# Performance work log

Measured on AMD Instinct MI355X. Metric: run time of the kernel, lower is better.

The kernel has to match this reference:

```python
import jax, jax.numpy as jnp
import numpy as np

DIM, HEADS, K = 128, 4, 7
HD = DIM // HEADS


def _nbr_idx(n, k):
    # NATTEN boundary-clamped neighborhood (dilation=1): window start clamped to [0, n-k]
    i = np.arange(n)
    start = np.clip(i - k // 2, 0, n - k)
    idx = start[:, None] + np.arange(k)[None, :]          # (n, k) absolute neighbor index
    rel = idx - i[:, None] + (k - 1)                      # (n, k) index into 2k-1 rpb axis
    return jnp.asarray(idx), jnp.asarray(rel)


def _ln(x, w, b, eps=1e-5):
    mu = jnp.mean(x, -1, keepdims=True)
    var = jnp.var(x, -1, keepdims=True)
    return (x - mu) * jax.lax.rsqrt(var + eps) * w + b


def setup_inputs() -> dict:
    key = jax.random.key(0)
    ks = jax.random.split(key, 16)
    B, H, W, C = 1, 128, 128, DIM
    f = jax.random.normal
    inp = {
        'x': f(ks[0], (B, H, W, C), jnp.float32),
        'y': f(ks[1], (B, H, W, C), jnp.float32),
        'qv_w': f(ks[2], (2 * C, C), jnp.float32) * 0.02,
        'qv_b': jnp.zeros((2 * C,), jnp.float32),
        'k_w': f(ks[3], (C, C), jnp.float32) * 0.02,
        'k_b': jnp.zeros((C,), jnp.float32),
        'rpb': f(ks[4], (HEADS, 2 * K - 1, 2 * K - 1), jnp.float32) * 0.02,
        'proj_w': f(ks[5], (C, C), jnp.float32) * 0.02,
        'proj_b': jnp.zeros((C,), jnp.float32),
        'n1_w': jnp.ones((C,), jnp.float32),
        'n1_b': jnp.zeros((C,), jnp.float32),
        'n2_w': jnp.ones((C,), jnp.float32),
        'n2_b': jnp.zeros((C,), jnp.float32),
        'fc1_w': f(ks[6], (4 * C, C), jnp.float32) * 0.02,
        'fc1_b': jnp.zeros((4 * C,), jnp.float32),
        'fc2_w': f(ks[7], (C, 4 * C), jnp.float32) * 0.02,
        'fc2_b': jnp.zeros((C,), jnp.float32),
    }
    return inp


def _block(x, y, qv_w, qv_b, k_w, k_b, rpb, proj_w, proj_b,
           n1_w, n1_b, n2_w, n2_b, fc1_w, fc1_b, fc2_w, fc2_b):
    B, H, W, C = x.shape
    scale = HD ** -0.5
    # ---- CrossNat2D attention on norm1(x) vs y ----
    xn = _ln(x, n1_w, n1_b)
    qv = xn @ qv_w.T + qv_b                               # (B,H,W,2C)
    q = qv[..., :C].reshape(B, H, W, HEADS, HD) * scale
    v = qv[..., C:].reshape(B, H, W, HEADS, HD)
    k = (y @ k_w.T + k_b).reshape(B, H, W, HEADS, HD)

    idx_h, rel_h = _nbr_idx(H, K)
    idx_w, rel_w = _nbr_idx(W, K)
    # gather neighborhoods: (B, H, K, W, K, HEADS, HD)
    k_nbr = k[:, idx_h][:, :, :, idx_w]
    v_nbr = v[:, idx_h][:, :, :, idx_w]

    # attention logits over KxK neighborhood
    attn = jnp.einsum('bijhd,biajchd->bijhac', q, k_nbr)  # (B,H,W,heads,K,K)
    bias = rpb[:, rel_h][..., rel_w]                      # (heads,H,K,W,K)
    attn = attn + jnp.transpose(bias, (1, 3, 0, 2, 4))    # broadcast over B
    attn = jax.nn.softmax(attn.reshape(B, H, W, HEADS, K * K), axis=-1)
    attn = attn.reshape(B, H, W, HEADS, K, K)

    out = jnp.einsum('bijhac,biajchd->bijhd', attn, v_nbr).reshape(B, H, W, C)
    out = out @ proj_w.T + proj_b

    x = x + out
    # ---- MLP ----
    h = _ln(x, n2_w, n2_b) @ fc1_w.T + fc1_b
    h = jax.nn.gelu(h, approximate=False) @ fc2_w.T + fc2_b
    return x + h


def reference(x, y, qv_w, qv_b, k_w, k_b, rpb, proj_w, proj_b,
              n1_w, n1_b, n2_w, n2_b, fc1_w, fc1_b, fc2_w, fc2_b):
    return _block(x, y, qv_w, qv_b, k_w, k_b, rpb, proj_w, proj_b,
                  n1_w, n1_b, n2_w, n2_b, fc1_w, fc1_b, fc2_w, fc2_b)
```

## Files before the change

### kernel.cpp

```cpp
#include <hip/hip_runtime.h>
#include <hip/hip_bf16.h>


#define N_PIX 16384
#define C 128
#define HEADS 4
#define HD 32
#define HW 128

typedef __hip_bfloat16 bf16;
typedef __attribute__((ext_vector_type(8))) short bf16x8;
typedef __attribute__((ext_vector_type(4))) float f32x4;

__device__ __forceinline__ short f2bs(float f) {
    unsigned int r;
    asm("v_cvt_pk_bf16_f32 %0, %1, %2" : "=v"(r) : "v"(f), "v"(f));
    return (short)(r & 0xffff);
}
__device__ __forceinline__ unsigned int pack2(float a, float b) {
    unsigned int r;
    asm("v_cvt_pk_bf16_f32 %0, %1, %2" : "=v"(r) : "v"(a), "v"(b));
    return r;
}
__device__ __forceinline__ float bs2f(short s) {
    __hip_bfloat16_raw r; r.x = (unsigned short)s;
    return __bfloat162float(__hip_bfloat16(r));
}
__device__ __forceinline__ float gelu_f(float v) {
    const float z2 = v * (2.302236206f + 0.102943322f * v * v);
    return v / (1.f + exp2f(-z2));
}

__global__ __launch_bounds__(256) void k_wconv(
    const float* __restrict__ qv_w, const float* __restrict__ k_w,
    const float* __restrict__ proj_w, const float* __restrict__ fc1_w,
    const float* __restrict__ fc2_w,
    short* __restrict__ wqv, short* __restrict__ wk, short* __restrict__ wproj,
    short* __restrict__ wfc1, short* __restrict__ wfc2) {
    const int i = blockIdx.x * 256 + threadIdx.x;
    if (i < 32768) wqv[i] = f2bs(qv_w[i]);
    if (i < 16384) { wk[i] = f2bs(k_w[i]); wproj[i] = f2bs(proj_w[i]); }
    if (i < 65536) { wfc1[i] = f2bs(fc1_w[i]); wfc2[i] = f2bs(fc2_w[i]); }
}

__global__ __launch_bounds__(256, 4) void k_qkv(
    const float* __restrict__ x, const float* __restrict__ y,
    const short* __restrict__ wqv, const float* __restrict__ qv_b,
    const short* __restrict__ wk, const float* __restrict__ k_b,
    const float* __restrict__ n1_w, const float* __restrict__ n1_b,
    bf16* __restrict__ qb, bf16* __restrict__ vb, bf16* __restrict__ kb) {
    __shared__ short xn[16][136];
    __shared__ short yl[16][136];
    const int t = threadIdx.x;
    const int pix0 = (blockIdx.x & 7) * 2048 + (blockIdx.x >> 3) * 16;
    {
        const int r = t >> 4, ch8 = (t & 15) * 8;
        const size_t gp = (size_t)(pix0 + r) * C + ch8;
        float xv[8], yv[8];
        *(float4*)&xv[0] = *(const float4*)(x + gp);
        *(float4*)&xv[4] = *(const float4*)(x + gp + 4);
        *(float4*)&yv[0] = *(const float4*)(y + gp);
        *(float4*)&yv[4] = *(const float4*)(y + gp + 4);
        float sm = 0.f, sq = 0.f;
#pragma unroll
        for (int i2 = 0; i2 < 8; i2++) { sm += xv[i2]; sq += xv[i2] * xv[i2]; }
#pragma unroll
        for (int msk = 1; msk < 16; msk <<= 1) {
            sm += __shfl_xor(sm, msk, 64); sq += __shfl_xor(sq, msk, 64);
        }
        const float mu = sm * (1.f / 128.f);
        const float ri = rsqrtf(sq * (1.f / 128.f) - mu * mu + 1e-5f);
        float w1[8], b1[8];
        *(float4*)&w1[0] = *(const float4*)(n1_w + ch8);
        *(float4*)&w1[4] = *(const float4*)(n1_w + ch8 + 4);
        *(float4*)&b1[0] = *(const float4*)(n1_b + ch8);
        *(float4*)&b1[4] = *(const float4*)(n1_b + ch8 + 4);
        uint4 xp, yp;
        xp.x = pack2((xv[0] - mu) * ri * w1[0] + b1[0], (xv[1] - mu) * ri * w1[1] + b1[1]);
        xp.y = pack2((xv[2] - mu) * ri * w1[2] + b1[2], (xv[3] - mu) * ri * w1[3] + b1[3]);
        xp.z = pack2((xv[4] - mu) * ri * w1[4] + b1[4], (xv[5] - mu) * ri * w1[5] + b1[5]);
        xp.w = pack2((xv[6] - mu) * ri * w1[6] + b1[6], (xv[7] - mu) * ri * w1[7] + b1[7]);
        yp.x = pack2(yv[0], yv[1]); yp.y = pack2(yv[2], yv[3]);
        yp.z = pack2(yv[4], yv[5]); yp.w = pack2(yv[6], yv[7]);
        *(uint4*)&xn[r][ch8] = xp;
        *(uint4*)&yl[r][ch8] = yp;
    }
    __syncthreads();
    const int wave = t >> 6, lane = t & 63, quad = lane >> 4, l15 = lane & 15;
    const float scale = 0.1767766952966369f;
    {
        bf16x8 aA[4];
#pragma unroll
        for (int kt = 0; kt < 4; kt++)
            aA[kt] = *(const bf16x8*)&xn[l15][kt * 32 + quad * 8];
#pragma unroll
        for (int s = 0; s < 4; s++) {
            const int n = (wave + 4 * s) * 16 + l15;
            f32x4 acc = {0.f, 0.f, 0.f, 0.f};
#pragma unroll
            for (int kt = 0; kt < 4; kt++) {
                bf16x8 b = *(const bf16x8*)&wqv[n * C + kt * 32 + quad * 8];
                acc = __builtin_amdgcn_mfma_f32_16x16x32_bf16(aA[kt], b, acc, 0, 0, 0);
            }
            const float bias = qv_b[n];
#pragma unroll
            for (int r = 0; r < 4; r++) {
                const int m = quad * 4 + r;
                const float v = acc[r] + bias;
                if (s < 2) qb[(size_t)(pix0 + m) * C + n] = __float2bfloat16(v * scale);
                else       vb[(size_t)(pix0 + m) * C + (n - C)] = __float2bfloat16(v);
            }
        }
    }
    {
        bf16x8 aY[4];
#pragma unroll
        for (int kt = 0; kt < 4; kt++)
            aY[kt] = *(const bf16x8*)&yl[l15][kt * 32 + quad * 8];
        const int n0 = (wave * 2) * 16 + l15, n1 = (wave * 2 + 1) * 16 + l15;
        f32x4 a0 = {0.f, 0.f, 0.f, 0.f}, a1 = {0.f, 0.f, 0.f, 0.f};
#pragma unroll
        for (int kt = 0; kt < 4; kt++) {
            bf16x8 b0 = *(const bf16x8*)&wk[n0 * C + kt * 32 + quad * 8];
            bf16x8 b1 = *(const bf16x8*)&wk[n1 * C + kt * 32 + quad * 8];
            a0 = __builtin_amdgcn_mfma_f32_16x16x32_bf16(aY[kt], b0, a0, 0, 0, 0);
            a1 = __builtin_amdgcn_mfma_f32_16x16x32_bf16(aY[kt], b1, a1, 0, 0, 0);
        }
        const float b0s = k_b[n0], b1s = k_b[n1];
#pragma unroll
        for (int r = 0; r < 4; r++) {
            const int m = quad * 4 + r;
            kb[(size_t)(pix0 + m) * C + n0] = __float2bfloat16(a0[r] + b0s);
            kb[(size_t)(pix0 + m) * C + n1] = __float2bfloat16(a1[r] + b1s);
        }
    }
}

__global__ __launch_bounds__(512, 2) void k_fam(
    const bf16* __restrict__ qb, const bf16* __restrict__ kb,
    const bf16* __restrict__ vb, const float* __restrict__ rpb,
    const float* __restrict__ x,
    const short* __restrict__ wproj, const float* __restrict__ proj_b,
    const float* __restrict__ n2_w, const float* __restrict__ n2_b,
    const short* __restrict__ wfc1, const float* __restrict__ fc1_b,
    const short* __restrict__ wfc2, const float* __restrict__ fc2_b,
    float* __restrict__ out) {
    __shared__ short SH[67104];
    short* const KU  = SH;
    short* const VU  = SH + 25872;
    short* const Pb  = SH + 51744;
    short* const aoL = SH;
    short* const xnb = SH + 8448;
    short* const hb  = SH + 16896;
    short* const x1b = SH + 51744;
    const int t = threadIdx.x;
    const int wave = t >> 6, lane = t & 63, quad = lane >> 4, l15 = lane & 15;
    const int h = wave & 3, mt = wave >> 2;
    const int p = wave & 1, g = wave >> 1;
    const int tile = (blockIdx.x & 7) * 32 + (blockIdx.x >> 3);
    const int i0 = (tile >> 4) * 8, j0 = (tile & 15) * 8;
    const int rs = min(max(i0 - 3, 0), 114);
    const int cs2 = min(max(j0 - 3, 0), 114);
    const int n_0 = (2 * g) * 16 + l15, n_1 = (2 * g + 1) * 16 + l15;
    bf16x8 aQv[2];
#pragma unroll
    for (int u = 0; u < 2; u++) {
        const int q = mt * 2 + u;
        const int iq = i0 + (q >> 1) * 4, jq = j0 + (q & 1) * 4;
        const int pA = (iq + (l15 >> 2)) * HW + jq + (l15 & 3);
        aQv[u] = *(const bf16x8*)(qb + (size_t)pA * C + h * HD + quad * 8);
    }
    float xres[2][2][4];
#pragma unroll
    for (int u = 0; u < 2; u++) {
        const int qm = 2 * p + u;
        const int ib = i0 + (qm >> 1) * 4 + quad, jb = j0 + (qm & 1) * 4;
#pragma unroll
        for (int r = 0; r < 4; r++) {
            const size_t pp = (size_t)(ib * HW + jb + r) * C;
            xres[u][0][r] = x[pp + n_0];
            xres[u][1][r] = x[pp + n_1];
        }
    }
    {
        const int seg = t & 15, r0 = t >> 4;
        int q14 = (r0 >= 28) ? 2 : (r0 >= 14 ? 1 : 0);
        int m14 = r0 - 14 * q14;
        int r = r0;
#pragma unroll
        for (int it = 0; it < 7; it++) {
            if (r < 196) {
                const size_t gp = (size_t)((rs + q14) * HW + (cs2 + m14)) * C + seg * 8;
                *(uint4*)&KU[r * 132 + seg * 8] = *(const uint4*)(kb + gp);
                *(uint4*)&VU[r * 132 + seg * 8] = *(const uint4*)(vb + gp);
            }
            r += 32; q14 += 2; m14 += 4;
            if (m14 >= 14) { m14 -= 14; q14 += 1; }
        }
    }
    int nrA[7], ncA[7];
    {
        int nr = (l15 >= 10) ? 1 : 0;
        int nc = l15 - ((l15 >= 10) ? 10 : 0);
#pragma unroll
        for (int nt = 0; nt < 7; nt++) {
            nrA[nt] = nr; ncA[nt] = nc;
            nc += 6; nr += 1;
            if (nc >= 10) { nc -= 10; nr += 1; }
        }
    }
    __syncthreads();
    const float* rpbh = rpb + h * 169;
    f32x4 Oacc[2][2];
#pragma unroll
    for (int u = 0; u < 2; u++) {
        Oacc[u][0] = (f32x4){0.f, 0.f, 0.f, 0.f};
        Oacc[u][1] = (f32x4){0.f, 0.f, 0.f, 0.f};
    }
#pragma unroll
    for (int u = 0; u < 2; u++) {
        const int q = mt * 2 + u;
        const int iq = i0 + (q >> 1) * 4, jq = j0 + (q & 1) * 4;
        const int rq = min(max(iq - 3, 0), 118), cq = min(max(jq - 3, 0), 118);
        const int vbase = (rq - rs) * 14 + (cq - cs2);
        f32x4 S[7];
#pragma unroll
        for (int nt = 0; nt < 7; nt++) {
            const int lr = min(vbase + nrA[nt] * 14 + ncA[nt], 195);
            const bf16x8 bK = *(const bf16x8*)&KU[lr * 132 + h * HD + quad * 8];
            f32x4 z = {0.f, 0.f, 0.f, 0.f};
            S[nt] = __builtin_amdgcn_mfma_f32_16x16x32_bf16(aQv[u], bK, z, 0, 0, 0);
        }
        float smx[4];
#pragma unroll
        for (int r = 0; r < 4; r++) {
            const int i = iq + quad, j = jq + r;
            const int shi = min(max(i - 3, 0), 121);
            const int swj = min(max(j - 3, 0), 121);
            float best = -1e30f;
#pragma unroll
            for (int nt = 0; nt < 7; nt++) {
                const int ai = rq + nrA[nt], aj = cq + ncA[nt];
                const bool vnb = (nt < 6) | (l15 < 4);
                const bool valid = vnb & (ai >= shi) & (ai <= shi + 6) & (aj >= swj) & (aj <= swj + 6);
                const int ri = min(max(ai - i + 6, 0), 12);
                const int rj = min(max(aj - j + 6, 0), 12);
                const float v = valid ? (S[nt][r] + rpbh[ri * 13 + rj]) : -1e30f;
                S[nt][r] = v;
                best = fmaxf(best, v);
            }
            for (int msk = 1; msk < 16; msk <<= 1) best = fmaxf(best, __shfl_xor(best, msk, 64));
            float s = 0.f;
#pragma unroll
            for (int nt = 0; nt < 7; nt++) {
                const float e = __expf(S[nt][r] - best);
                S[nt][r] = e;
                s += e;
            }
            for (int msk = 1; msk < 16; msk <<= 1) s += __shfl_xor(s, msk, 64);
            smx[r] = 1.f / s;
        }
#pragma unroll
        for (int r = 0; r < 4; r++) {
            short* prow = &Pb[(wave * 16 + quad * 4 + r) * 120];
#pragma unroll
            for (int nt = 0; nt < 7; nt++)
                prow[nt * 16 + l15] = f2bs(S[nt][r] * smx[r]);
        }
#pragma unroll
        for (int kt = 0; kt < 3; kt++) {
            const bf16x8 aP = *(const bf16x8*)&Pb[(wave * 16 + l15) * 120 + kt * 32 + quad * 8];
            const int kbase = kt * 32 + quad * 8;
            int kr = (kbase * 205) >> 11;
            int kc = kbase - 10 * kr;
            int sidx = vbase + kr * 14 + kc;
            int lvr[8];
#pragma unroll
            for (int jj = 0; jj < 8; jj++) {
                lvr[jj] = sidx;
                kc++; sidx++;
                if (kc >= 10) { kc = 0; sidx += 4; }
            }
#pragma unroll
            for (int nt2 = 0; nt2 < 2; nt2++) {
                const int ch = h * HD + nt2 * 16 + l15;
                bf16x8 bV;
#pragma unroll
                for (int jj = 0; jj < 8; jj++) bV[jj] = VU[lvr[jj] * 132 + ch];
                Oacc[u][nt2] = __builtin_amdgcn_mfma_f32_16x16x32_bf16(aP, bV, Oacc[u][nt2], 0, 0, 0);
            }
        }
        {
            bf16x8 aP = {0, 0, 0, 0, 0, 0, 0, 0};
            if (quad < 2) aP = *(const bf16x8*)&Pb[(wave * 16 + l15) * 120 + 96 + quad * 8];
#pragma unroll
            for (int nt2 = 0; nt2 < 2; nt2++) {
                const int ch = h * HD + nt2 * 16 + l15;
                bf16x8 bV = {0, 0, 0, 0, 0, 0, 0, 0};
                if (quad == 0) {
#pragma unroll
                    for (int jj = 0; jj < 8; jj++) {
                        const int kc3 = (6 + jj > 9) ? 9 : 6 + jj;
                        bV[jj] = VU[(vbase + 126 + kc3) * 132 + ch];
                    }
                }
                Oacc[u][nt2] = __builtin_amdgcn_mfma_f32_16x16x32_bf16(aP, bV, Oacc[u][nt2], 0, 0, 0);
            }
        }
    }
    bf16x8 wp0[4], wp1[4];
#pragma unroll
    for (int kt = 0; kt < 4; kt++) {
        wp0[kt] = *(const bf16x8*)&wproj[n_0 * C + kt * 32 + quad * 8];
        wp1[kt] = *(const bf16x8*)&wproj[n_1 * C + kt * 32 + quad * 8];
    }
    __syncthreads();
#pragma unroll
    for (int u = 0; u < 2; u++) {
        const int q = mt * 2 + u;
#pragma unroll
        for (int r = 0; r < 4; r++) {
            const int m = q * 16 + quad * 4 + r;
            aoL[m * 132 + h * HD + l15] = f2bs(Oacc[u][0][r]);
            aoL[m * 132 + h * HD + 16 + l15] = f2bs(Oacc[u][1][r]);
        }
    }
    __syncthreads();
    float x1f[2][2][4];
    {
        bf16x8 aO[2][4];
#pragma unroll
        for (int u = 0; u < 2; u++)
#pragma unroll
            for (int kt = 0; kt < 4; kt++)
                aO[u][kt] = *(const bf16x8*)&aoL[((2 * p + u) * 16 + l15) * 132 + kt * 32 + quad * 8];
        f32x4 pa[2][2];
        pa[0][0] = (f32x4){0.f, 0.f, 0.f, 0.f}; pa[0][1] = (f32x4){0.f, 0.f, 0.f, 0.f};
        pa[1][0] = (f32x4){0.f, 0.f, 0.f, 0.f}; pa[1][1] = (f32x4){0.f, 0.f, 0.f, 0.f};
#pragma unroll
        for (int kt = 0; kt < 4; kt++) {
            pa[0][0] = __builtin_amdgcn_mfma_f32_16x16x32_bf16(aO[0][kt], wp0[kt], pa[0][0], 0, 0, 0);
            pa[0][1] = __builtin_amdgcn_mfma_f32_16x16x32_bf16(aO[0][kt], wp1[kt], pa[0][1], 0, 0, 0);
            pa[1][0] = __builtin_amdgcn_mfma_f32_16x16x32_bf16(aO[1][kt], wp0[kt], pa[1][0], 0, 0, 0);
            pa[1][1] = __builtin_amdgcn_mfma_f32_16x16x32_bf16(aO[1][kt], wp1[kt], pa[1][1], 0, 0, 0);
        }
        const float b0s = proj_b[n_0], b1s = proj_b[n_1];
#pragma unroll
        for (int u = 0; u < 2; u++) {
#pragma unroll
            for (int r = 0; r < 4; r++) {
                const int m = (2 * p + u) * 16 + quad * 4 + r;
                const float v0 = xres[u][0][r] + pa[u][0][r] + b0s;
                const float v1 = xres[u][1][r] + pa[u][1][r] + b1s;
                x1f[u][0][r] = v0; x1f[u][1][r] = v1;
                x1b[m * 132 + n_0] = f2bs(v0);
                x1b[m * 132 + n_1] = f2bs(v1);
            }
        }
    }
    __syncthreads();
    {
        const int row = t >> 3, c16 = (t & 7) * 16;
        float xv[16];
        {
            const uint4 d0 = *(const uint4*)&x1b[row * 132 + c16];
            const uint4 d1 = *(const uint4*)&x1b[row * 132 + c16 + 8];
            const unsigned int w[8] = {d0.x, d0.y, d0.z, d0.w, d1.x, d1.y, d1.z, d1.w};
#pragma unroll
            for (int i2 = 0; i2 < 8; i2++) {
                xv[2 * i2]     = bs2f((short)(w[i2] & 0xffff));
                xv[2 * i2 + 1] = bs2f((short)(w[i2] >> 16));
            }
        }
        float sm = 0.f, sq = 0.f;
#pragma unroll
        for (int i2 = 0; i2 < 16; i2++) { sm += xv[i2]; sq += xv[i2] * xv[i2]; }
#pragma unroll
        for (int msk = 1; msk < 8; msk <<= 1) {
            sm += __shfl_xor(sm, msk, 64); sq += __shfl_xor(sq, msk, 64);
        }
        const float mu = sm * (1.f / 128.f);
        const float ri = rsqrtf(sq * (1.f / 128.f) - mu * mu + 1e-5f);
        float w2[16], b2[16];
        *(float4*)&w2[0]  = *(const float4*)(n2_w + c16);
        *(float4*)&w2[4]  = *(const float4*)(n2_w + c16 + 4);
        *(float4*)&w2[8]  = *(const float4*)(n2_w + c16 + 8);
        *(float4*)&w2[12] = *(const float4*)(n2_w + c16 + 12);
        *(float4*)&b2[0]  = *(const float4*)(n2_b + c16);
        *(float4*)&b2[4]  = *(const float4*)(n2_b + c16 + 4);
        *(float4*)&b2[8]  = *(const float4*)(n2_b + c16 + 8);
        *(float4*)&b2[12] = *(const float4*)(n2_b + c16 + 12);
        uint4 o0, o1;
        o0.x = pack2((xv[0] - mu) * ri * w2[0] + b2[0],   (xv[1] - mu) * ri * w2[1] + b2[1]);
        o0.y = pack2((xv[2] - mu) * ri * w2[2] + b2[2],   (xv[3] - mu) * ri * w2[3] + b2[3]);
        o0.z = pack2((xv[4] - mu) * ri * w2[4] + b2[4],   (xv[5] - mu) * ri * w2[5] + b2[5]);
        o0.w = pack2((xv[6] - mu) * ri * w2[6] + b2[6],   (xv[7] - mu) * ri * w2[7] + b2[7]);
        o1.x = pack2((xv[8] - mu) * ri * w2[8] + b2[8],   (xv[9] - mu) * ri * w2[9] + b2[9]);
        o1.y = pack2((xv[10] - mu) * ri * w2[10] + b2[10], (xv[11] - mu) * ri * w2[11] + b2[11]);
        o1.z = pack2((xv[12] - mu) * ri * w2[12] + b2[12], (xv[13] - mu) * ri * w2[13] + b2[13]);
        o1.w = pack2((xv[14] - mu) * ri * w2[14] + b2[14], (xv[15] - mu) * ri * w2[15] + b2[15]);
        *(uint4*)&xnb[row * 132 + c16] = o0;
        *(uint4*)&xnb[row * 132 + c16 + 8] = o1;
    }
    __syncthreads();
    {
        bf16x8 aX[2][4];
#pragma unroll
        for (int u = 0; u < 2; u++)
#pragma unroll
            for (int kt = 0; kt < 4; kt++)
                aX[u][kt] = *(const bf16x8*)&xnb[((2 * p + u) * 16 + l15) * 132 + kt * 32 + quad * 8];
#pragma unroll
        for (int a = 0; a < 8; a++) {
            const int n = (g * 8 + a) * 16 + l15;
            f32x4 c0 = {0.f, 0.f, 0.f, 0.f}, c1 = {0.f, 0.f, 0.f, 0.f};
#pragma unroll
            for (int kt = 0; kt < 4; kt++) {
                const bf16x8 bw = *(const bf16x8*)&wfc1[n * C + kt * 32 + quad * 8];
                c0 = __builtin_amdgcn_mfma_f32_16x16x32_bf16(aX[0][kt], bw, c0, 0, 0, 0);
                c1 = __builtin_amdgcn_mfma_f32_16x16x32_bf16(aX[1][kt], bw, c1, 0, 0, 0);
            }
            const float bias = fc1_b[n];
#pragma unroll
            for (int r = 0; r < 4; r++) {
                const int m0 = (2 * p) * 16 + quad * 4 + r;
                hb[m0 * 520 + n] = f2bs(gelu_f(c0[r] + bias));
                hb[(m0 + 16) * 520 + n] = f2bs(gelu_f(c1[r] + bias));
            }
        }
    }
    __syncthreads();
    {
        f32x4 f00 = {0.f, 0.f, 0.f, 0.f}, f01 = {0.f, 0.f, 0.f, 0.f};
        f32x4 f10 = {0.f, 0.f, 0.f, 0.f}, f11 = {0.f, 0.f, 0.f, 0.f};
#pragma unroll
        for (int kt = 0; kt < 16; kt++) {
            const bf16x8 a0 = *(const bf16x8*)&hb[((2 * p) * 16 + l15) * 520 + kt * 32 + quad * 8];
            const bf16x8 a1 = *(const bf16x8*)&hb[((2 * p + 1) * 16 + l15) * 520 + kt * 32 + quad * 8];
            const bf16x8 w0 = *(const bf16x8*)&wfc2[n_0 * 512 + kt * 32 + quad * 8];
            const bf16x8 w1 = *(const bf16x8*)&wfc2[n_1 * 512 + kt * 32 + quad * 8];
            f00 = __builtin_amdgcn_mfma_f32_16x16x32_bf16(a0, w0, f00, 0, 0, 0);
            f01 = __builtin_amdgcn_mfma_f32_16x16x32_bf16(a0, w1, f01, 0, 0, 0);
            f10 = __builtin_amdgcn_mfma_f32_16x16x32_bf16(a1, w0, f10, 0, 0, 0);
            f11 = __builtin_amdgcn_mfma_f32_16x16x32_bf16(a1, w1, f11, 0, 0, 0);
        }
        const float b0s = fc2_b[n_0], b1s = fc2_b[n_1];
#pragma unroll
        for (int u = 0; u < 2; u++) {
            const int qm = 2 * p + u;
            const int ib = i0 + (qm >> 1) * 4 + quad, jb = j0 + (qm & 1) * 4;
#pragma unroll
            for (int r = 0; r < 4; r++) {
                const size_t pp = (size_t)(ib * HW + jb + r) * C;
                const float v0 = (u ? f10[r] : f00[r]) + b0s + x1f[u][0][r];
                const float v1 = (u ? f11[r] : f01[r]) + b1s + x1f[u][1][r];
                out[pp + n_0] = v0;
                out[pp + n_1] = v1;
            }
        }
    }
}

extern "C" void kernel_launch(void* const* d_in, const int* in_sizes, int n_in,
                              void* d_out, int out_size, void* d_ws, size_t ws_size,
                              hipStream_t stream) {
    const float* x      = (const float*)d_in[0];
    const float* y      = (const float*)d_in[1];
    const float* qv_w   = (const float*)d_in[2];
    const float* qv_b   = (const float*)d_in[3];
    const float* k_w    = (const float*)d_in[4];
    const float* k_b    = (const float*)d_in[5];
    const float* rpb    = (const float*)d_in[6];
    const float* proj_w = (const float*)d_in[7];
    const float* proj_b = (const float*)d_in[8];
    const float* n1_w   = (const float*)d_in[9];
    const float* n1_b   = (const float*)d_in[10];
    const float* n2_w   = (const float*)d_in[11];
    const float* n2_b   = (const float*)d_in[12];
    const float* fc1_w  = (const float*)d_in[13];
    const float* fc1_b  = (const float*)d_in[14];
    const float* fc2_w  = (const float*)d_in[15];
    const float* fc2_b  = (const float*)d_in[16];
    float* out = (float*)d_out;

    bf16* qb  = (bf16*)d_ws;
    bf16* vb  = qb + (size_t)N_PIX * C;
    bf16* kb  = vb + (size_t)N_PIX * C;
    short* wqv  = (short*)(kb + (size_t)N_PIX * C);
    short* wk   = wqv + 32768;
    short* wproj= wk + 16384;
    short* wfc1 = wproj + 16384;
    short* wfc2 = wfc1 + 65536;

    k_wconv<<<256, 256, 0, stream>>>(qv_w, k_w, proj_w, fc1_w, fc2_w,
                                     wqv, wk, wproj, wfc1, wfc2);
    k_qkv<<<1024, 256, 0, stream>>>(x, y, wqv, qv_b, wk, k_b, n1_w, n1_b,
                                    qb, vb, kb);
    k_fam<<<256, 512, 0, stream>>>(qb, kb, vb, rpb, x, wproj, proj_b, n2_w, n2_b,
                                   wfc1, fc1_b, wfc2, fc2_b, out);
}
```

Before: 152.6 us.

## Enlarge QKV projection tile to 64 pixels per block with register weight reuse

The QKV kernel now processes 64 pixels per 512-thread block instead of 16 per 256 threads. Each wave loads its weight column fragments once and reuses them across four 16-row M tiles, which cuts redundant global weight loads per pixel. Grid size drops from 1024 to 256 blocks, so there are fewer waves to hide latency and register pressure rises from holding 16 A-fragments per wave.

```diff
diff --git a/kernel.cpp b/kernel.cpp
--- a/kernel.cpp
+++ b/kernel.cpp
@@ -43,96 +43,134 @@
     if (i < 65536) { wfc1[i] = f2bs(fc1_w[i]); wfc2[i] = f2bs(fc2_w[i]); }
 }
 
-__global__ __launch_bounds__(256, 4) void k_qkv(
+__global__ __launch_bounds__(512, 4) void k_qkv(
     const float* __restrict__ x, const float* __restrict__ y,
     const short* __restrict__ wqv, const float* __restrict__ qv_b,
     const short* __restrict__ wk, const float* __restrict__ k_b,
     const float* __restrict__ n1_w, const float* __restrict__ n1_b,
     bf16* __restrict__ qb, bf16* __restrict__ vb, bf16* __restrict__ kb) {
-    __shared__ short xn[16][136];
-    __shared__ short yl[16][136];
+    __shared__ short xn[64][136];
+    __shared__ short yl[64][136];
     const int t = threadIdx.x;
-    const int pix0 = (blockIdx.x & 7) * 2048 + (blockIdx.x >> 3) * 16;
-    {
-        const int r = t >> 4, ch8 = (t & 15) * 8;
-        const size_t gp = (size_t)(pix0 + r) * C + ch8;
-        float xv[8], yv[8];
-        *(float4*)&xv[0] = *(const float4*)(x + gp);
-        *(float4*)&xv[4] = *(const float4*)(x + gp + 4);
-        *(float4*)&yv[0] = *(const float4*)(y + gp);
-        *(float4*)&yv[4] = *(const float4*)(y + gp + 4);
+    const int pix0 = ((blockIdx.x & 7) * 32 + (blockIdx.x >> 3)) * 64;
+    {
+        const int r = t >> 3, c16 = (t & 7) * 16;
+        const size_t gp = (size_t)(pix0 + r) * C + c16;
+        float xv[16], yv[16];
+        *(float4*)&xv[0]  = *(const float4*)(x + gp);
+        *(float4*)&xv[4]  = *(const float4*)(x + gp + 4);
+        *(float4*)&xv[8]  = *(const float4*)(x + gp + 8);
+        *(float4*)&xv[12] = *(const float4*)(x + gp + 12);
+        *(float4*)&yv[0]  = *(const float4*)(y + gp);
+        *(float4*)&yv[4]  = *(const float4*)(y + gp + 4);
+        *(float4*)&yv[8]  = *(const float4*)(y + gp + 8);
+        *(float4*)&yv[12] = *(const float4*)(y + gp + 12);
         float sm = 0.f, sq = 0.f;
 #pragma unroll
-        for (int i2 = 0; i2 < 8; i2++) { sm += xv[i2]; sq += xv[i2] * xv[i2]; }
-#pragma unroll
-        for (int msk = 1; msk < 16; msk <<= 1) {
+        for (int i2 = 0; i2 < 16; i2++) { sm += xv[i2]; sq += xv[i2] * xv[i2]; }
+#pragma unroll
+        for (int msk = 1; msk < 8; msk <<= 1) {
             sm += __shfl_xor(sm, msk, 64); sq += __shfl_xor(sq, msk, 64);
         }
         const float mu = sm * (1.f / 128.f);
         const float ri = rsqrtf(sq * (1.f / 128.f) - mu * mu + 1e-5f);
-        float w1[8], b1[8];
-        *(float4*)&w1[0] = *(const float4*)(n1_w + ch8);
-        *(float4*)&w1[4] = *(const float4*)(n1_w + ch8 + 4);
-        *(float4*)&b1[0] = *(const float4*)(n1_b + ch8);
-        *(float4*)&b1[4] = *(const float4*)(n1_b + ch8 + 4);
-        uint4 xp, yp;
-        xp.x = pack2((xv[0] - mu) * ri * w1[0] + b1[0], (xv[1] - mu) * ri * w1[1] + b1[1]);
-        xp.y = pack2((xv[2] - mu) * ri * w1[2] + b1[2], (xv[3] - mu) * ri * w1[3] + b1[3]);
-        xp.z = pack2((xv[4] - mu) * ri * w1[4] + b1[4], (xv[5] - mu) * ri * w1[5] + b1[5]);
-        xp.w = pack2((xv[6] - mu) * ri * w1[6] + b1[6], (xv[7] - mu) * ri * w1[7] + b1[7]);
-        yp.x = pack2(yv[0], yv[1]); yp.y = pack2(yv[2], yv[3]);
-        yp.z = pack2(yv[4], yv[5]); yp.w = pack2(yv[6], yv[7]);
-        *(uint4*)&xn[r][ch8] = xp;
-        *(uint4*)&yl[r][ch8] = yp;
+        float w1[16], b1[16];
+        *(float4*)&w1[0]  = *(const float4*)(n1_w + c16);
+        *(float4*)&w1[4]  = *(const float4*)(n1_w + c16 + 4);
+        *(float4*)&w1[8]  = *(const float4*)(n1_w + c16 + 8);
+        *(float4*)&w1[12] = *(const float4*)(n1_w + c16 + 12);
+        *(float4*)&b1[0]  = *(const float4*)(n1_b + c16);
+        *(float4*)&b1[4]  = *(const float4*)(n1_b + c16 + 4);
+        *(float4*)&b1[8]  = *(const float4*)(n1_b + c16 + 8);
+        *(float4*)&b1[12] = *(const float4*)(n1_b + c16 + 12);
+        uint4 o0, o1, p0, p1;
+        o0.x = pack2((xv[0] - mu) * ri * w1[0] + b1[0],   (xv[1] - mu) * ri * w1[1] + b1[1]);
+        o0.y = pack2((xv[2] - mu) * ri * w1[2] + b1[2],   (xv[3] - mu) * ri * w1[3] + b1[3]);
+        o0.z = pack2((xv[4] - mu) * ri * w1[4] + b1[4],   (xv[5] - mu) * ri * w1[5] + b1[5]);
+        o0.w = pack2((xv[6] - mu) * ri * w1[6] + b1[6],   (xv[7] - mu) * ri * w1[7] + b1[7]);
+        o1.x = pack2((xv[8] - mu) * ri * w1[8] + b1[8],   (xv[9] - mu) * ri * w1[9] + b1[9]);
+        o1.y = pack2((xv[10] - mu) * ri * w1[10] + b1[10], (xv[11] - mu) * ri * w1[11] + b1[11]);
+        o1.z = pack2((xv[12] - mu) * ri * w1[12] + b1[12], (xv[13] - mu) * ri * w1[13] + b1[13]);
+        o1.w = pack2((xv[14] - mu) * ri * w1[14] + b1[14], (xv[15] - mu) * ri * w1[15] + b1[15]);
+        p0.x = pack2(yv[0], yv[1]);   p0.y = pack2(yv[2], yv[3]);
+        p0.z = pack2(yv[4], yv[5]);   p0.w = pack2(yv[6], yv[7]);
+        p1.x = pack2(yv[8], yv[9]);   p1.y = pack2(yv[10], yv[11]);
+        p1.z = pack2(yv[12], yv[13]); p1.w = pack2(yv[14], yv[15]);
+        *(uint4*)&xn[r][c16] = o0;
+        *(uint4*)&xn[r][c16 + 8] = o1;
+        *(uint4*)&yl[r][c16] = p0;
+        *(uint4*)&yl[r][c16 + 8] = p1;
     }
     __syncthreads();
     const int wave = t >> 6, lane = t & 63, quad = lane >> 4, l15 = lane & 15;
     const float scale = 0.1767766952966369f;
     {
-        bf16x8 aA[4];
+        bf16x8 aA[4][4];
+#pragma unroll
+        for (int m = 0; m < 4; m++)
+#pragma unroll
+            for (int kt = 0; kt < 4; kt++)
+                aA[m][kt] = *(const bf16x8*)&xn[m * 16 + l15][kt * 32 + quad * 8];
+#pragma unroll
+        for (int s = 0; s < 2; s++) {
+            const int n = (wave * 2 + s) * 16 + l15;
+            bf16x8 w[4];
+#pragma unroll
+            for (int kt = 0; kt < 4; kt++)
+                w[kt] = *(const bf16x8*)&wqv[n * C + kt * 32 + quad * 8];
+            f32x4 acc[4];
+#pragma unroll
+            for (int m = 0; m < 4; m++) acc[m] = (f32x4){0.f, 0.f, 0.f, 0.f};
+#pragma unroll
+            for (int m = 0; m < 4; m++)
+#pragma unroll
+                for (int kt = 0; kt < 4; kt++)
+                    acc[m] = __builtin_amdgcn_mfma_f32_16x16x32_bf16(aA[m][kt], w[kt], acc[m], 0, 0, 0);
+            const float bias = qv_b[n];
+            if (wave * 2 + s < 8) {
+#pragma unroll
+                for (int m = 0; m < 4; m++)
+#pragma unroll
+                    for (int r = 0; r < 4; r++)
+                        qb[(size_t)(pix0 + m * 16 + quad * 4 + r) * C + n] =
+                            __float2bfloat16((acc[m][r] + bias) * scale);
+            } else {
+#pragma unroll
+                for (int m = 0; m < 4; m++)
+#pragma unroll
+                    for (int r = 0; r < 4; r++)
+                        vb[(size_t)(pix0 + m * 16 + quad * 4 + r) * C + (n - C)] =
+                            __float2bfloat16(acc[m][r] + bias);
+            }
+        }
+    }
+    {
+        bf16x8 aY[4][4];
+#pragma unroll
+        for (int m = 0; m < 4; m++)
+#pragma unroll
+            for (int kt = 0; kt < 4; kt++)
+                aY[m][kt] = *(const bf16x8*)&yl[m * 16 + l15][kt * 32 + quad * 8];
+        const int n = wave * 16 + l15;
+        bf16x8 w[4];
 #pragma unroll
         for (int kt = 0; kt < 4; kt++)
-            aA[kt] = *(const bf16x8*)&xn[l15][kt * 32 + quad * 8];
-#pragma unroll
-        for (int s = 0; s < 4; s++) {
-            const int n = (wave + 4 * s) * 16 + l15;
-            f32x4 acc = {0.f, 0.f, 0.f, 0.f};
-#pragma unroll
-            for (int kt = 0; kt < 4; kt++) {
-                bf16x8 b = *(const bf16x8*)&wqv[n * C + kt * 32 + quad * 8];
-                acc = __builtin_amdgcn_mfma_f32_16x16x32_bf16(aA[kt], b, acc, 0, 0, 0);
-            }
-            const float bias = qv_b[n];
-#pragma unroll
-            for (int r = 0; r < 4; r++) {
-                const int m = quad * 4 + r;
-                const float v = acc[r] + bias;
-                if (s < 2) qb[(size_t)(pix0 + m) * C + n] = __float2bfloat16(v * scale);
-                else       vb[(size_t)(pix0 + m) * C + (n - C)] = __float2bfloat16(v);
-            }
-        }
-    }
-    {
-        bf16x8 aY[4];
-#pragma unroll
-        for (int kt = 0; kt < 4; kt++)
-            aY[kt] = *(const bf16x8*)&yl[l15][kt * 32 + quad * 8];
-        const int n0 = (wave * 2) * 16 + l15, n1 = (wave * 2 + 1) * 16 + l15;
-        f32x4 a0 = {0.f, 0.f, 0.f, 0.f}, a1 = {0.f, 0.f, 0.f, 0.f};
-#pragma unroll
-        for (int kt = 0; kt < 4; kt++) {
-            bf16x8 b0 = *(const bf16x8*)&wk[n0 * C + kt * 32 + quad * 8];
-            bf16x8 b1 = *(const bf16x8*)&wk[n1 * C + kt * 32 + quad * 8];
-            a0 = __builtin_amdgcn_mfma_f32_16x16x32_bf16(aY[kt], b0, a0, 0, 0, 0);
-            a1 = __builtin_amdgcn_mfma_f32_16x16x32_bf16(aY[kt], b1, a1, 0, 0, 0);
-        }
-        const float b0s = k_b[n0], b1s = k_b[n1];
-#pragma unroll
-        for (int r = 0; r < 4; r++) {
-            const int m = quad * 4 + r;
-            kb[(size_t)(pix0 + m) * C + n0] = __float2bfloat16(a0[r] + b0s);
-            kb[(size_t)(pix0 + m) * C + n1] = __float2bfloat16(a1[r] + b1s);
-        }
+            w[kt] = *(const bf16x8*)&wk[n * C + kt * 32 + quad * 8];
+        f32x4 acc[4];
+#pragma unroll
+        for (int m = 0; m < 4; m++) acc[m] = (f32x4){0.f, 0.f, 0.f, 0.f};
+#pragma unroll
+        for (int m = 0; m < 4; m++)
+#pragma unroll
+            for (int kt = 0; kt < 4; kt++)
+                acc[m] = __builtin_amdgcn_mfma_f32_16x16x32_bf16(aY[m][kt], w[kt], acc[m], 0, 0, 0);
+        const float bias = k_b[n];
+#pragma unroll
+        for (int m = 0; m < 4; m++)
+#pragma unroll
+            for (int r = 0; r < 4; r++)
+                kb[(size_t)(pix0 + m * 16 + quad * 4 + r) * C + n] =
+                    __float2bfloat16(acc[m][r] + bias);
     }
 }
 
@@ -494,8 +532,8 @@
 
     k_wconv<<<256, 256, 0, stream>>>(qv_w, k_w, proj_w, fc1_w, fc2_w,
                                      wqv, wk, wproj, wfc1, wfc2);
-    k_qkv<<<1024, 256, 0, stream>>>(x, y, wqv, qv_b, wk, k_b, n1_w, n1_b,
-                                    qb, vb, kb);
+    k_qkv<<<256, 512, 0, stream>>>(x, y, wqv, qv_b, wk, k_b, n1_w, n1_b,
+                                   qb, vb, kb);
     k_fam<<<256, 512, 0, stream>>>(qb, kb, vb, rpb, x, wproj, proj_b, n2_w, n2_b,
                                    wfc1, fc1_b, wfc2, fc2_b, out);
 }
```

Result: faster. 146.3 us, median of 2 (-4.1%).
